# Kernel tuning notes

Hardware: AMD Instinct MI355X
Metric: run time of the kernel (lower is better)

The kernel has to match this reference:

```python
import jax, jax.numpy as jnp
import numpy as np
from jax import lax

C, HID, NCLS, CDIM = 16, 128, 32, 64

def _dwconv(x, k):
    # x: [B,C,H,W], k: [C,1,3,3] depthwise (groups=C), SAME padding
    return lax.conv_general_dilated(
        x, k, window_strides=(1, 1), padding='SAME',
        dimension_numbers=('NCHW', 'OIHW', 'NCHW'), feature_group_count=x.shape[1])

def setup_inputs() -> dict:
    key = jax.random.key(0)
    ks = jax.random.split(key, 10)
    B, H, W = 4, 256, 256
    Fin = 3 * C
    inp = {
        'x': jax.random.normal(ks[0], (B, C, H, W), jnp.float32),
        'cond': jax.random.randint(ks[1], (B,), 0, NCLS, jnp.int32),
        'embed': jax.random.normal(ks[2], (NCLS, CDIM), jnp.float32) * 0.1,
        # Linear weights stored as [in, out] (transposed torch layout)
        'film_w': jax.random.normal(ks[3], (CDIM, 2 * HID), jnp.float32) * (1.0 / np.sqrt(CDIM)),
        'film_b': jnp.zeros((2 * HID,), jnp.float32),
        'fc1_w': jax.random.normal(ks[4], (Fin, HID), jnp.float32) * (1.0 / np.sqrt(Fin)),
        'fc1_b': jnp.zeros((HID,), jnp.float32),
        'fc2_w': jax.random.normal(ks[5], (HID, HID), jnp.float32) * (1.0 / np.sqrt(HID)),
        'fc2_b': jnp.zeros((HID,), jnp.float32),
        # fc3 is zero-init in the module; use small random values so output != input
        'fc3_w': jax.random.normal(ks[6], (HID, C), jnp.float32) * 0.01,
        'fc3_b': jnp.zeros((C,), jnp.float32),
        'n_steps': 4,
    }
    return inp

def reference(x, cond, embed, film_w, film_b, fc1_w, fc1_b, fc2_w, fc2_b, fc3_w, fc3_b, n_steps):
    sx = jnp.array([[-1., 0., 1.], [-2., 0., 2.], [-1., 0., 1.]], jnp.float32)
    kx = jnp.tile(sx[None, None], (C, 1, 1, 1))   # [C,1,3,3]
    ky = jnp.tile(sx.T[None, None], (C, 1, 1, 1))

    # FiLM params are step-invariant: compute once
    film = embed[cond] @ film_w + film_b          # [B, 2*HID]
    gamma, beta = jnp.split(film, 2, axis=1)      # [B, HID] each
    gamma = gamma[:, None, None, :]               # [B,1,1,HID]
    beta = beta[:, None, None, :]

    def step(xs, _):
        gx = _dwconv(xs, kx)
        gy = _dwconv(xs, ky)
        feats = jnp.concatenate([xs, gx, gy], axis=1).transpose(0, 2, 3, 1)  # [B,H,W,3C]
        h = jax.nn.relu(feats @ fc1_w + fc1_b)
        h = gamma * h + beta
        h = jax.nn.relu(h @ fc2_w + fc2_b)
        dx = (h @ fc3_w + fc3_b).transpose(0, 3, 1, 2)                        # [B,C,H,W]
        dx = jnp.clip(dx, -10.0, 10.0)
        return xs + dx * 0.1, None

    out, _ = lax.scan(step, x, None, length=n_steps)
    return out
```

## Files before the change

### kernel.cpp

```cpp
#include <hip/hip_runtime.h>

typedef __bf16 bf16x8 __attribute__((ext_vector_type(8)));
typedef float f32x4 __attribute__((ext_vector_type(4)));
typedef float f32x16 __attribute__((ext_vector_type(16)));
typedef unsigned int u32x4 __attribute__((ext_vector_type(4)));

#define FILM_WS 0
#define W1_WS   4096
#define W2B_WS  20480
#define W3_WS   151552
#define B2_WS   159744
#define XBUF_WS 163840

#define W1_OFF  0
#define W2_OFF  16384
#define W3_OFF  49152
#define B2_OFF  57344
#define XL_OFF  57856
#define LDS_TOTAL 92672

static __device__ __forceinline__ unsigned short f2bf(float f) {
  unsigned int u = __builtin_bit_cast(unsigned int, f);
  u += 0x7fffu + ((u >> 16) & 1u);
  return (unsigned short)(u >> 16);
}

static __device__ __forceinline__ unsigned cvtpk(float lo, float hi) {
  unsigned r;
  asm("v_cvt_pk_bf16_f32 %0, %1, %2" : "=v"(r) : "v"(lo), "v"(hi));
  return r;
}

static __device__ __forceinline__ void plswap(unsigned &a, unsigned &b) {
  auto r = __builtin_amdgcn_permlane32_swap((int)a, (int)b, false, false);
  a = (unsigned)r[0];
  b = (unsigned)r[1];
}

__global__ __launch_bounds__(256) void prep_film(
    const int* __restrict__ cond, const float* __restrict__ embed,
    const float* __restrict__ film_w, const float* __restrict__ film_b,
    char* __restrict__ ws) {
  int id = blockIdx.x * 256 + threadIdx.x;
  int b = id >> 8, j = id & 255;
  const float* e = embed + cond[b] * 64;
  float s = film_b[j];
  #pragma unroll 8
  for (int k = 0; k < 64; ++k) s += e[k] * film_w[k * 256 + j];
  ((float*)(ws + FILM_WS))[b * 256 + j] = s;
}

__global__ __launch_bounds__(256) void prep_w(
    const float* __restrict__ fc1w, const float* __restrict__ fc1b,
    const float* __restrict__ fc2w, const float* __restrict__ fc2b,
    const float* __restrict__ fc3w, char* __restrict__ ws) {
  int id = blockIdx.x * 256 + threadIdx.x;
  const float* film = (const float*)(ws + FILM_WS);
  if (id < 8192) {
    int n = id >> 6, k = id & 63;
    float v = (k < 48) ? fc1w[k * 128 + n] : (k == 48 ? fc1b[n] : 0.f);
    *(unsigned short*)(ws + W1_WS + ((n * 128 + 2 * k) ^ ((n & 7) << 4))) = f2bf(v);
  } else if (id < 8192 + 65536) {
    int t = id - 8192; int bb = t >> 14; t &= 16383;
    int n = t >> 7, k = t & 127;
    float v = film[bb * 256 + k] * fc2w[k * 128 + n];
    *(unsigned short*)(ws + W2B_WS + bb * 32768 + ((n * 256 + 2 * k) ^ ((n & 15) << 4))) = f2bf(v);
  } else if (id < 8192 + 65536 + 4096) {
    int t = id - 73728; int n = t >> 7, k = t & 127;
    float v = (n < 16) ? fc3w[k * 16 + n] : 0.f;
    *(unsigned short*)(ws + W3_WS + ((n * 256 + 2 * k) ^ ((n & 15) << 4))) = f2bf(v);
  } else if (id < 8192 + 65536 + 4096 + 512) {
    int t = id - 77824; int bb = t >> 7, n = t & 127;
    float s = fc2b[n];
    for (int k = 0; k < 128; ++k)
      s += film[bb * 256 + 128 + k] * fc2w[k * 128 + n];
    ((float*)(ws + B2_WS))[bb * 128 + n] = s;
  }
}

__global__ __launch_bounds__(512, 2) void step_kernel(
    const float* __restrict__ xin, float* __restrict__ xout,
    const char* __restrict__ ws, const float* __restrict__ fc3b) {
  extern __shared__ char sm[];
  float* smf = (float*)(sm + XL_OFF);
  const int tid = threadIdx.x;
  const int bid = blockIdx.x;
  const int b = bid >> 6, idx = bid & 63;

  for (int i = tid; i < 3584; i += 512) {
    const char* src; int dst;
    if (i < 1024)      { src = ws + W1_WS + i * 16;                       dst = W1_OFF + i * 16; }
    else if (i < 3072) { src = ws + W2B_WS + b * 32768 + (i - 1024) * 16; dst = W2_OFF + (i - 1024) * 16; }
    else               { src = ws + W3_WS + (i - 3072) * 16;              dst = W3_OFF + (i - 3072) * 16; }
    *(u32x4*)(sm + dst) = *(const u32x4*)src;
  }
  if (tid < 128)
    ((float*)(sm + B2_OFF))[tid] = ((const float*)(ws + B2_WS + b * 512))[tid];

  const int lane = tid & 63, wv = tid >> 6;
  const int l31 = lane & 31, h5 = lane >> 5;
  const int band = wv * 32;
  const int p = band + l31, pr = p >> 7, pcol = p & 127;
  const int cbase = h5 * 8;
  const float b3v = (l31 < 16) ? fc3b[l31] : 0.f;
  const unsigned bONE = (h5 == 0) ? 0x3F80u : 0u;
  const bf16x8 fone = __builtin_bit_cast(bf16x8, (u32x4){bONE, 0u, 0u, 0u});

  const int iseg = tid >> 5, iq = tid & 31;
  const int eseg = tid >> 1, ee = tid & 1;

  f32x4 pre[4];
  float peg = 0.f;
  {
    const int h0 = idx * 4;
    #pragma unroll
    for (int k = 0; k < 4; ++k) {
      int seg = iseg + k * 16;
      int c = seg >> 2, dh = seg & 3;
      int g = h0 - 1 + dh;
      pre[k] = (f32x4){0.f, 0.f, 0.f, 0.f};
      if ((unsigned)g < 256u)
        pre[k] = *(const f32x4*)(xin + (((b * 16 + c) * 256 + g) << 8) + 4 * iq);
    }
    if (tid < 128) {
      int c = eseg >> 2, dh = eseg & 3;
      int g = h0 - 1 + dh;
      int w = -1 + ee * 129;
      if ((unsigned)g < 256u && (unsigned)w < 256u)
        peg = xin[(((b * 16 + c) * 256 + g) << 8) + w];
    }
  }

  for (int j = 0; j < 4; ++j) {
    const int h0 = idx * 4 + (j >> 1) * 2;
    const int w0 = (j & 1) << 7;
    __syncthreads();
    #pragma unroll
    for (int k = 0; k < 4; ++k)
      *(f32x4*)(smf + (iseg + k * 16) * 136 + 4 + 4 * iq) = pre[k];
    if (tid < 128)
      smf[eseg * 136 + 3 + ee * 129] = peg;
    __syncthreads();

    if (j < 3) {
      const int nh0 = idx * 4 + ((j + 1) >> 1) * 2;
      const int nw0 = ((j + 1) & 1) << 7;
      #pragma unroll
      for (int k = 0; k < 4; ++k) {
        int seg = iseg + k * 16;
        int c = seg >> 2, dh = seg & 3;
        int g = nh0 - 1 + dh;
        pre[k] = (f32x4){0.f, 0.f, 0.f, 0.f};
        if ((unsigned)g < 256u)
          pre[k] = *(const f32x4*)(xin + (((b * 16 + c) * 256 + g) << 8) + nw0 + 4 * iq);
      }
      peg = 0.f;
      if (tid < 128) {
        int c = eseg >> 2, dh = eseg & 3;
        int g = nh0 - 1 + dh;
        int w = nw0 - 1 + ee * 129;
        if ((unsigned)g < 256u && (unsigned)w < 256u)
          peg = xin[(((b * 16 + c) * 256 + g) << 8) + w];
      }
    }

    bf16x8 fx, fgx, fgy;
    #pragma unroll
    for (int jc = 0; jc < 8; ++jc) {
      const float* s0 = smf + ((cbase + jc) * 4 + pr) * 136 + 3 + pcol;
      float a00 = s0[0],   a01 = s0[1],   a02 = s0[2];
      float a10 = s0[136], a11 = s0[137], a12 = s0[138];
      float a20 = s0[272], a21 = s0[273], a22 = s0[274];
      fx[jc]  = (__bf16)a11;
      fgx[jc] = (__bf16)((a02 - a00) + 2.f * (a12 - a10) + (a22 - a20));
      fgy[jc] = (__bf16)((a20 - a00) + 2.f * (a21 - a01) + (a22 - a02));
    }

    f32x16 acc1[4];
    #pragma unroll
    for (int nt = 0; nt < 4; ++nt) {
      const int n = nt * 32 + l31;
      const int rb = n * 128, sw = (n & 7) << 4;
      bf16x8 wA = __builtin_bit_cast(bf16x8, *(const u32x4*)(sm + W1_OFF + ((rb +  0 + 16 * h5) ^ sw)));
      bf16x8 wB = __builtin_bit_cast(bf16x8, *(const u32x4*)(sm + W1_OFF + ((rb + 32 + 16 * h5) ^ sw)));
      bf16x8 wC = __builtin_bit_cast(bf16x8, *(const u32x4*)(sm + W1_OFF + ((rb + 64 + 16 * h5) ^ sw)));
      bf16x8 wD = __builtin_bit_cast(bf16x8, *(const u32x4*)(sm + W1_OFF + ((rb + 96 + 16 * h5) ^ sw)));
      f32x16 a = (f32x16){0.f,0.f,0.f,0.f,0.f,0.f,0.f,0.f,0.f,0.f,0.f,0.f,0.f,0.f,0.f,0.f};
      a = __builtin_amdgcn_mfma_f32_32x32x16_bf16(wA, fx,   a, 0, 0, 0);
      a = __builtin_amdgcn_mfma_f32_32x32x16_bf16(wB, fgx,  a, 0, 0, 0);
      a = __builtin_amdgcn_mfma_f32_32x32x16_bf16(wC, fgy,  a, 0, 0, 0);
      a = __builtin_amdgcn_mfma_f32_32x32x16_bf16(wD, fone, a, 0, 0, 0);
      acc1[nt] = a;
    }

    unsigned zf[8][4];
    #pragma unroll
    for (int kk = 0; kk < 8; ++kk) {
      const int Qa = 2 * kk, Qb = 2 * kk + 1;
      unsigned A0 = cvtpk(fmaxf(acc1[Qa >> 2][(Qa & 3) * 4 + 0], 0.f),
                          fmaxf(acc1[Qa >> 2][(Qa & 3) * 4 + 1], 0.f));
      unsigned A1 = cvtpk(fmaxf(acc1[Qa >> 2][(Qa & 3) * 4 + 2], 0.f),
                          fmaxf(acc1[Qa >> 2][(Qa & 3) * 4 + 3], 0.f));
      unsigned B0 = cvtpk(fmaxf(acc1[Qb >> 2][(Qb & 3) * 4 + 0], 0.f),
                          fmaxf(acc1[Qb >> 2][(Qb & 3) * 4 + 1], 0.f));
      unsigned B1 = cvtpk(fmaxf(acc1[Qb >> 2][(Qb & 3) * 4 + 2], 0.f),
                          fmaxf(acc1[Qb >> 2][(Qb & 3) * 4 + 3], 0.f));
      plswap(A0, B0); plswap(A1, B1);
      zf[kk][0] = A0; zf[kk][1] = A1; zf[kk][2] = B0; zf[kk][3] = B1;
    }

    float bv[4];
    #pragma unroll
    for (int nt = 0; nt < 4; ++nt)
      bv[nt] = ((const float*)(sm + B2_OFF))[nt * 32 + l31];
    f32x16 acc2[4];
    #pragma unroll
    for (int nt = 0; nt < 4; ++nt) {
      const int n = nt * 32 + l31;
      const int rb = n * 256, sw = (n & 15) << 4;
      f32x16 a = (f32x16){0.f,0.f,0.f,0.f,0.f,0.f,0.f,0.f,0.f,0.f,0.f,0.f,0.f,0.f,0.f,0.f};
      #pragma unroll
      for (int kk = 0; kk < 8; ++kk) {
        bf16x8 wf = __builtin_bit_cast(bf16x8,
            *(const u32x4*)(sm + W2_OFF + ((rb + 32 * kk + 16 * h5) ^ sw)));
        bf16x8 zk = __builtin_bit_cast(bf16x8,
            (u32x4){zf[kk][0], zf[kk][1], zf[kk][2], zf[kk][3]});
        a = __builtin_amdgcn_mfma_f32_32x32x16_bf16(wf, zk, a, 0, 0, 0);
      }
      bf16x8 wb = __builtin_bit_cast(bf16x8,
          (u32x4){(h5 == 0) ? cvtpk(bv[nt], 0.f) : 0u, 0u, 0u, 0u});
      a = __builtin_amdgcn_mfma_f32_32x32x16_bf16(wb, fone, a, 0, 0, 0);
      acc2[nt] = a;
    }

    unsigned hf[8][4];
    #pragma unroll
    for (int kk = 0; kk < 8; ++kk) {
      const int Qa = 2 * kk, Qb = 2 * kk + 1;
      unsigned A0 = cvtpk(fmaxf(acc2[Qa >> 2][(Qa & 3) * 4 + 0], 0.f),
                          fmaxf(acc2[Qa >> 2][(Qa & 3) * 4 + 1], 0.f));
      unsigned A1 = cvtpk(fmaxf(acc2[Qa >> 2][(Qa & 3) * 4 + 2], 0.f),
                          fmaxf(acc2[Qa >> 2][(Qa & 3) * 4 + 3], 0.f));
      unsigned B0 = cvtpk(fmaxf(acc2[Qb >> 2][(Qb & 3) * 4 + 0], 0.f),
                          fmaxf(acc2[Qb >> 2][(Qb & 3) * 4 + 1], 0.f));
      unsigned B1 = cvtpk(fmaxf(acc2[Qb >> 2][(Qb & 3) * 4 + 2], 0.f),
                          fmaxf(acc2[Qb >> 2][(Qb & 3) * 4 + 3], 0.f));
      plswap(A0, B0); plswap(A1, B1);
      hf[kk][0] = A0; hf[kk][1] = A1; hf[kk][2] = B0; hf[kk][3] = B1;
    }

    f32x16 a3 = (f32x16){0.f,0.f,0.f,0.f,0.f,0.f,0.f,0.f,0.f,0.f,0.f,0.f,0.f,0.f,0.f,0.f};
    {
      const int rb = l31 * 256, sw = (l31 & 15) << 4;
      #pragma unroll
      for (int kk = 0; kk < 8; ++kk) {
        bf16x8 wf = __builtin_bit_cast(bf16x8,
            *(const u32x4*)(sm + W3_OFF + ((rb + 32 * kk + 16 * h5) ^ sw)));
        bf16x8 hk = __builtin_bit_cast(bf16x8,
            (u32x4){hf[kk][0], hf[kk][1], hf[kk][2], hf[kk][3]});
        a3 = __builtin_amdgcn_mfma_f32_32x32x16_bf16(wf, hk, a3, 0, 0, 0);
      }
      bf16x8 wb = __builtin_bit_cast(bf16x8,
          (u32x4){(h5 == 0) ? cvtpk(b3v, 0.f) : 0u, 0u, 0u, 0u});
      a3 = __builtin_amdgcn_mfma_f32_32x32x16_bf16(wb, fone, a3, 0, 0, 0);
    }

    #pragma unroll
    for (int r = 0; r < 8; ++r) {
      const int c = 4 * h5 + (r & 3) + 8 * (r >> 2);
      float dx = a3[r];
      dx = fminf(fmaxf(dx, -10.f), 10.f);
      float xold = smf[(c * 4 + pr + 1) * 136 + 4 + pcol];
      xout[(((b * 16 + c) * 256 + h0 + pr) << 8) + w0 + pcol] = xold + 0.1f * dx;
    }
  }
}

extern "C" void kernel_launch(void* const* d_in, const int* in_sizes, int n_in,
                              void* d_out, int out_size, void* d_ws, size_t ws_size,
                              hipStream_t stream) {
  const float* x      = (const float*)d_in[0];
  const int*   cond   = (const int*)d_in[1];
  const float* embed  = (const float*)d_in[2];
  const float* film_w = (const float*)d_in[3];
  const float* film_b = (const float*)d_in[4];
  const float* fc1w   = (const float*)d_in[5];
  const float* fc1b   = (const float*)d_in[6];
  const float* fc2w   = (const float*)d_in[7];
  const float* fc2b   = (const float*)d_in[8];
  const float* fc3w   = (const float*)d_in[9];
  const float* fc3b   = (const float*)d_in[10];

  char*  ws   = (char*)d_ws;
  float* xbuf = (float*)(ws + XBUF_WS);
  float* out  = (float*)d_out;

  prep_film<<<4, 256, 0, stream>>>(cond, embed, film_w, film_b, ws);
  prep_w<<<306, 256, 0, stream>>>(fc1w, fc1b, fc2w, fc2b, fc3w, ws);

  dim3 grid(256), blk(512);
  step_kernel<<<grid, blk, LDS_TOTAL, stream>>>(x,    xbuf, ws, fc3b);
  step_kernel<<<grid, blk, LDS_TOTAL, stream>>>(xbuf, out,  ws, fc3b);
  step_kernel<<<grid, blk, LDS_TOTAL, stream>>>(out,  xbuf, ws, fc3b);
  step_kernel<<<grid, blk, LDS_TOTAL, stream>>>(xbuf, out,  ws, fc3b);
}
```

Baseline: 107.5 us.

## Process two pixel tiles per wave with a taller 6-row halo tile

Each wave now handles 64 pixels as two 32-pixel MFMA column tiles, so every weight fragment loaded from LDS feeds two MFMAs. The block tile is 4 rows by 128 columns with a 6-row halo, processed in two passes instead of four passes of 2 rows, which cuts redundant halo loads and barriers. The bias values move from LDS into registers preloaded once, and the accumulator-to-bf16 conversion is interleaved per n-tile. In exchange, LDS grows to about 107 KB and register pressure roughly doubles, which may limit occupancy under the 2-blocks-per-CU launch bound.

After: 178.3 us. 1.66x slower.

```diff
diff --git a/kernel.cpp b/kernel.cpp
--- a/kernel.cpp
+++ b/kernel.cpp
@@ -15,9 +15,8 @@
 #define W1_OFF  0
 #define W2_OFF  16384
 #define W3_OFF  49152
-#define B2_OFF  57344
-#define XL_OFF  57856
-#define LDS_TOTAL 92672
+#define XL_OFF  57344
+#define LDS_TOTAL 109568
 
 static __device__ __forceinline__ unsigned short f2bf(float f) {
   unsigned int u = __builtin_bit_cast(unsigned int, f);
@@ -36,6 +35,23 @@
   a = (unsigned)r[0];
   b = (unsigned)r[1];
 }
+
+#define CVTSTORE(Z, nt, a) do {                                          \
+    unsigned A0 = cvtpk(fmaxf((a)[0], 0.f),  fmaxf((a)[1], 0.f));        \
+    unsigned A1 = cvtpk(fmaxf((a)[2], 0.f),  fmaxf((a)[3], 0.f));        \
+    unsigned B0 = cvtpk(fmaxf((a)[4], 0.f),  fmaxf((a)[5], 0.f));        \
+    unsigned B1 = cvtpk(fmaxf((a)[6], 0.f),  fmaxf((a)[7], 0.f));        \
+    plswap(A0, B0); plswap(A1, B1);                                      \
+    Z[2*(nt)][0] = A0; Z[2*(nt)][1] = A1; Z[2*(nt)][2] = B0; Z[2*(nt)][3] = B1; \
+    A0 = cvtpk(fmaxf((a)[8], 0.f),  fmaxf((a)[9], 0.f));                 \
+    A1 = cvtpk(fmaxf((a)[10], 0.f), fmaxf((a)[11], 0.f));                \
+    B0 = cvtpk(fmaxf((a)[12], 0.f), fmaxf((a)[13], 0.f));                \
+    B1 = cvtpk(fmaxf((a)[14], 0.f), fmaxf((a)[15], 0.f));                \
+    plswap(A0, B0); plswap(A1, B1);                                      \
+    Z[2*(nt)+1][0] = A0; Z[2*(nt)+1][1] = A1; Z[2*(nt)+1][2] = B0; Z[2*(nt)+1][3] = B1; \
+  } while (0)
+
+#define ZERO16 (f32x16){0.f,0.f,0.f,0.f,0.f,0.f,0.f,0.f,0.f,0.f,0.f,0.f,0.f,0.f,0.f,0.f}
 
 __global__ __launch_bounds__(256) void prep_film(
     const int* __restrict__ cond, const float* __restrict__ embed,
@@ -86,6 +102,7 @@
   const int tid = threadIdx.x;
   const int bid = blockIdx.x;
   const int b = bid >> 6, idx = bid & 63;
+  const int h0 = idx * 4;
 
   for (int i = tid; i < 3584; i += 512) {
     const char* src; int dst;
@@ -94,89 +111,90 @@
     else               { src = ws + W3_WS + (i - 3072) * 16;              dst = W3_OFF + (i - 3072) * 16; }
     *(u32x4*)(sm + dst) = *(const u32x4*)src;
   }
-  if (tid < 128)
-    ((float*)(sm + B2_OFF))[tid] = ((const float*)(ws + B2_WS + b * 512))[tid];
 
   const int lane = tid & 63, wv = tid >> 6;
   const int l31 = lane & 31, h5 = lane >> 5;
-  const int band = wv * 32;
-  const int p = band + l31, pr = p >> 7, pcol = p & 127;
+  const int band = wv * 64;
+  const int p0 = band + l31,      p1 = band + 32 + l31;
+  const int pr0 = p0 >> 7, pc0 = p0 & 127;
+  const int pr1 = p1 >> 7, pc1 = p1 & 127;
   const int cbase = h5 * 8;
-  const float b3v = (l31 < 16) ? fc3b[l31] : 0.f;
   const unsigned bONE = (h5 == 0) ? 0x3F80u : 0u;
   const bf16x8 fone = __builtin_bit_cast(bf16x8, (u32x4){bONE, 0u, 0u, 0u});
 
+  unsigned wb2[4];
+  #pragma unroll
+  for (int nt = 0; nt < 4; ++nt) {
+    float bvv = ((const float*)(ws + B2_WS))[b * 128 + nt * 32 + l31];
+    wb2[nt] = (h5 == 0) ? cvtpk(bvv, 0.f) : 0u;
+  }
+  const float b3v = (l31 < 16) ? fc3b[l31] : 0.f;
+  const unsigned wb3 = (h5 == 0) ? cvtpk(b3v, 0.f) : 0u;
+
   const int iseg = tid >> 5, iq = tid & 31;
   const int eseg = tid >> 1, ee = tid & 1;
 
-  f32x4 pre[4];
-  float peg = 0.f;
-  {
-    const int h0 = idx * 4;
-    #pragma unroll
-    for (int k = 0; k < 4; ++k) {
-      int seg = iseg + k * 16;
-      int c = seg >> 2, dh = seg & 3;
+  f32x4 pre[6];
+  float peg;
+  auto PREFETCH = [&](int w0p) {
+    #pragma unroll
+    for (int k = 0; k < 6; ++k) {
+      int seg = iseg + 16 * k;
+      int c = seg / 6, dh = seg - 6 * c;
       int g = h0 - 1 + dh;
       pre[k] = (f32x4){0.f, 0.f, 0.f, 0.f};
       if ((unsigned)g < 256u)
-        pre[k] = *(const f32x4*)(xin + (((b * 16 + c) * 256 + g) << 8) + 4 * iq);
-    }
-    if (tid < 128) {
-      int c = eseg >> 2, dh = eseg & 3;
+        pre[k] = *(const f32x4*)(xin + (((b * 16 + c) * 256 + g) << 8) + w0p + 4 * iq);
+    }
+    peg = 0.f;
+    if (tid < 192) {
+      int c = eseg / 6, dh = eseg - 6 * c;
       int g = h0 - 1 + dh;
-      int w = -1 + ee * 129;
+      int w = w0p - 1 + ee * 129;
       if ((unsigned)g < 256u && (unsigned)w < 256u)
         peg = xin[(((b * 16 + c) * 256 + g) << 8) + w];
     }
-  }
-
-  for (int j = 0; j < 4; ++j) {
-    const int h0 = idx * 4 + (j >> 1) * 2;
-    const int w0 = (j & 1) << 7;
+  };
+
+  PREFETCH(0);
+
+  #pragma unroll
+  for (int j = 0; j < 2; ++j) {
+    const int w0 = j << 7;
     __syncthreads();
     #pragma unroll
-    for (int k = 0; k < 4; ++k)
-      *(f32x4*)(smf + (iseg + k * 16) * 136 + 4 + 4 * iq) = pre[k];
-    if (tid < 128)
+    for (int k = 0; k < 6; ++k)
+      *(f32x4*)(smf + (iseg + 16 * k) * 136 + 4 + 4 * iq) = pre[k];
+    if (tid < 192)
       smf[eseg * 136 + 3 + ee * 129] = peg;
     __syncthreads();
 
-    if (j < 3) {
-      const int nh0 = idx * 4 + ((j + 1) >> 1) * 2;
-      const int nw0 = ((j + 1) & 1) << 7;
-      #pragma unroll
-      for (int k = 0; k < 4; ++k) {
-        int seg = iseg + k * 16;
-        int c = seg >> 2, dh = seg & 3;
-        int g = nh0 - 1 + dh;
-        pre[k] = (f32x4){0.f, 0.f, 0.f, 0.f};
-        if ((unsigned)g < 256u)
-          pre[k] = *(const f32x4*)(xin + (((b * 16 + c) * 256 + g) << 8) + nw0 + 4 * iq);
-      }
-      peg = 0.f;
-      if (tid < 128) {
-        int c = eseg >> 2, dh = eseg & 3;
-        int g = nh0 - 1 + dh;
-        int w = nw0 - 1 + ee * 129;
-        if ((unsigned)g < 256u && (unsigned)w < 256u)
-          peg = xin[(((b * 16 + c) * 256 + g) << 8) + w];
-      }
-    }
-
-    bf16x8 fx, fgx, fgy;
+    if (j == 0) PREFETCH(128);
+
+    bf16x8 fx0, fgx0, fgy0, fx1, fgx1, fgy1;
     #pragma unroll
     for (int jc = 0; jc < 8; ++jc) {
-      const float* s0 = smf + ((cbase + jc) * 4 + pr) * 136 + 3 + pcol;
-      float a00 = s0[0],   a01 = s0[1],   a02 = s0[2];
-      float a10 = s0[136], a11 = s0[137], a12 = s0[138];
-      float a20 = s0[272], a21 = s0[273], a22 = s0[274];
-      fx[jc]  = (__bf16)a11;
-      fgx[jc] = (__bf16)((a02 - a00) + 2.f * (a12 - a10) + (a22 - a20));
-      fgy[jc] = (__bf16)((a20 - a00) + 2.f * (a21 - a01) + (a22 - a02));
-    }
-
-    f32x16 acc1[4];
+      {
+        const float* s0 = smf + ((cbase + jc) * 6 + pr0) * 136 + 3 + pc0;
+        float a00 = s0[0],   a01 = s0[1],   a02 = s0[2];
+        float a10 = s0[136], a11 = s0[137], a12 = s0[138];
+        float a20 = s0[272], a21 = s0[273], a22 = s0[274];
+        fx0[jc]  = (__bf16)a11;
+        fgx0[jc] = (__bf16)((a02 - a00) + 2.f * (a12 - a10) + (a22 - a20));
+        fgy0[jc] = (__bf16)((a20 - a00) + 2.f * (a21 - a01) + (a22 - a02));
+      }
+      {
+        const float* s0 = smf + ((cbase + jc) * 6 + pr1) * 136 + 3 + pc1;
+        float a00 = s0[0],   a01 = s0[1],   a02 = s0[2];
+        float a10 = s0[136], a11 = s0[137], a12 = s0[138];
+        float a20 = s0[272], a21 = s0[273], a22 = s0[274];
+        fx1[jc]  = (__bf16)a11;
+        fgx1[jc] = (__bf16)((a02 - a00) + 2.f * (a12 - a10) + (a22 - a20));
+        fgy1[jc] = (__bf16)((a20 - a00) + 2.f * (a21 - a01) + (a22 - a02));
+      }
+    }
+
+    unsigned zf0[8][4], zf1[8][4];
     #pragma unroll
     for (int nt = 0; nt < 4; ++nt) {
       const int n = nt * 32 + l31;
@@ -185,93 +203,67 @@
       bf16x8 wB = __builtin_bit_cast(bf16x8, *(const u32x4*)(sm + W1_OFF + ((rb + 32 + 16 * h5) ^ sw)));
       bf16x8 wC = __builtin_bit_cast(bf16x8, *(const u32x4*)(sm + W1_OFF + ((rb + 64 + 16 * h5) ^ sw)));
       bf16x8 wD = __builtin_bit_cast(bf16x8, *(const u32x4*)(sm + W1_OFF + ((rb + 96 + 16 * h5) ^ sw)));
-      f32x16 a = (f32x16){0.f,0.f,0.f,0.f,0.f,0.f,0.f,0.f,0.f,0.f,0.f,0.f,0.f,0.f,0.f,0.f};
-      a = __builtin_amdgcn_mfma_f32_32x32x16_bf16(wA, fx,   a, 0, 0, 0);
-      a = __builtin_amdgcn_mfma_f32_32x32x16_bf16(wB, fgx,  a, 0, 0, 0);
-      a = __builtin_amdgcn_mfma_f32_32x32x16_bf16(wC, fgy,  a, 0, 0, 0);
-      a = __builtin_amdgcn_mfma_f32_32x32x16_bf16(wD, fone, a, 0, 0, 0);
-      acc1[nt] = a;
-    }
-
-    unsigned zf[8][4];
-    #pragma unroll
-    for (int kk = 0; kk < 8; ++kk) {
-      const int Qa = 2 * kk, Qb = 2 * kk + 1;
-      unsigned A0 = cvtpk(fmaxf(acc1[Qa >> 2][(Qa & 3) * 4 + 0], 0.f),
-                          fmaxf(acc1[Qa >> 2][(Qa & 3) * 4 + 1], 0.f));
-      unsigned A1 = cvtpk(fmaxf(acc1[Qa >> 2][(Qa & 3) * 4 + 2], 0.f),
-                          fmaxf(acc1[Qa >> 2][(Qa & 3) * 4 + 3], 0.f));
-      unsigned B0 = cvtpk(fmaxf(acc1[Qb >> 2][(Qb & 3) * 4 + 0], 0.f),
-                          fmaxf(acc1[Qb >> 2][(Qb & 3) * 4 + 1], 0.f));
-      unsigned B1 = cvtpk(fmaxf(acc1[Qb >> 2][(Qb & 3) * 4 + 2], 0.f),
-                          fmaxf(acc1[Qb >> 2][(Qb & 3) * 4 + 3], 0.f));
-      plswap(A0, B0); plswap(A1, B1);
-      zf[kk][0] = A0; zf[kk][1] = A1; zf[kk][2] = B0; zf[kk][3] = B1;
-    }
-
-    float bv[4];
-    #pragma unroll
-    for (int nt = 0; nt < 4; ++nt)
-      bv[nt] = ((const float*)(sm + B2_OFF))[nt * 32 + l31];
-    f32x16 acc2[4];
+      f32x16 a0 = ZERO16, a1 = ZERO16;
+      a0 = __builtin_amdgcn_mfma_f32_32x32x16_bf16(wA, fx0,  a0, 0, 0, 0);
+      a1 = __builtin_amdgcn_mfma_f32_32x32x16_bf16(wA, fx1,  a1, 0, 0, 0);
+      a0 = __builtin_amdgcn_mfma_f32_32x32x16_bf16(wB, fgx0, a0, 0, 0, 0);
+      a1 = __builtin_amdgcn_mfma_f32_32x32x16_bf16(wB, fgx1, a1, 0, 0, 0);
+      a0 = __builtin_amdgcn_mfma_f32_32x32x16_bf16(wC, fgy0, a0, 0, 0, 0);
+      a1 = __builtin_amdgcn_mfma_f32_32x32x16_bf16(wC, fgy1, a1, 0, 0, 0);
+      a0 = __builtin_amdgcn_mfma_f32_32x32x16_bf16(wD, fone, a0, 0, 0, 0);
+      a1 = __builtin_amdgcn_mfma_f32_32x32x16_bf16(wD, fone, a1, 0, 0, 0);
+      CVTSTORE(zf0, nt, a0);
+      CVTSTORE(zf1, nt, a1);
+    }
+
+    unsigned hf0[8][4], hf1[8][4];
     #pragma unroll
     for (int nt = 0; nt < 4; ++nt) {
       const int n = nt * 32 + l31;
       const int rb = n * 256, sw = (n & 15) << 4;
-      f32x16 a = (f32x16){0.f,0.f,0.f,0.f,0.f,0.f,0.f,0.f,0.f,0.f,0.f,0.f,0.f,0.f,0.f,0.f};
+      f32x16 a0 = ZERO16, a1 = ZERO16;
       #pragma unroll
       for (int kk = 0; kk < 8; ++kk) {
         bf16x8 wf = __builtin_bit_cast(bf16x8,
             *(const u32x4*)(sm + W2_OFF + ((rb + 32 * kk + 16 * h5) ^ sw)));
-        bf16x8 zk = __builtin_bit_cast(bf16x8,
-            (u32x4){zf[kk][0], zf[kk][1], zf[kk][2], zf[kk][3]});
-        a = __builtin_amdgcn_mfma_f32_32x32x16_bf16(wf, zk, a, 0, 0, 0);
-      }
-      bf16x8 wb = __builtin_bit_cast(bf16x8,
-          (u32x4){(h5 == 0) ? cvtpk(bv[nt], 0.f) : 0u, 0u, 0u, 0u});
-      a = __builtin_amdgcn_mfma_f32_32x32x16_bf16(wb, fone, a, 0, 0, 0);
-      acc2[nt] = a;
-    }
-
-    unsigned hf[8][4];
-    #pragma unroll
-    for (int kk = 0; kk < 8; ++kk) {
-      const int Qa = 2 * kk, Qb = 2 * kk + 1;
-      unsigned A0 = cvtpk(fmaxf(acc2[Qa >> 2][(Qa & 3) * 4 + 0], 0.f),
-                          fmaxf(acc2[Qa >> 2][(Qa & 3) * 4 + 1], 0.f));
-      unsigned A1 = cvtpk(fmaxf(acc2[Qa >> 2][(Qa & 3) * 4 + 2], 0.f),
-                          fmaxf(acc2[Qa >> 2][(Qa & 3) * 4 + 3], 0.f));
-      unsigned B0 = cvtpk(fmaxf(acc2[Qb >> 2][(Qb & 3) * 4 + 0], 0.f),
-                          fmaxf(acc2[Qb >> 2][(Qb & 3) * 4 + 1], 0.f));
-      unsigned B1 = cvtpk(fmaxf(acc2[Qb >> 2][(Qb & 3) * 4 + 2], 0.f),
-                          fmaxf(acc2[Qb >> 2][(Qb & 3) * 4 + 3], 0.f));
-      plswap(A0, B0); plswap(A1, B1);
-      hf[kk][0] = A0; hf[kk][1] = A1; hf[kk][2] = B0; hf[kk][3] = B1;
-    }
-
-    f32x16 a3 = (f32x16){0.f,0.f,0.f,0.f,0.f,0.f,0.f,0.f,0.f,0.f,0.f,0.f,0.f,0.f,0.f,0.f};
+        a0 = __builtin_amdgcn_mfma_f32_32x32x16_bf16(wf,
+            __builtin_bit_cast(bf16x8, (u32x4){zf0[kk][0], zf0[kk][1], zf0[kk][2], zf0[kk][3]}), a0, 0, 0, 0);
+        a1 = __builtin_amdgcn_mfma_f32_32x32x16_bf16(wf,
+            __builtin_bit_cast(bf16x8, (u32x4){zf1[kk][0], zf1[kk][1], zf1[kk][2], zf1[kk][3]}), a1, 0, 0, 0);
+      }
+      bf16x8 wbf = __builtin_bit_cast(bf16x8, (u32x4){wb2[nt], 0u, 0u, 0u});
+      a0 = __builtin_amdgcn_mfma_f32_32x32x16_bf16(wbf, fone, a0, 0, 0, 0);
+      a1 = __builtin_amdgcn_mfma_f32_32x32x16_bf16(wbf, fone, a1, 0, 0, 0);
+      CVTSTORE(hf0, nt, a0);
+      CVTSTORE(hf1, nt, a1);
+    }
+
+    f32x16 c0 = ZERO16, c1 = ZERO16;
     {
       const int rb = l31 * 256, sw = (l31 & 15) << 4;
       #pragma unroll
       for (int kk = 0; kk < 8; ++kk) {
         bf16x8 wf = __builtin_bit_cast(bf16x8,
             *(const u32x4*)(sm + W3_OFF + ((rb + 32 * kk + 16 * h5) ^ sw)));
-        bf16x8 hk = __builtin_bit_cast(bf16x8,
-            (u32x4){hf[kk][0], hf[kk][1], hf[kk][2], hf[kk][3]});
-        a3 = __builtin_amdgcn_mfma_f32_32x32x16_bf16(wf, hk, a3, 0, 0, 0);
-      }
-      bf16x8 wb = __builtin_bit_cast(bf16x8,
-          (u32x4){(h5 == 0) ? cvtpk(b3v, 0.f) : 0u, 0u, 0u, 0u});
-      a3 = __builtin_amdgcn_mfma_f32_32x32x16_bf16(wb, fone, a3, 0, 0, 0);
+        c0 = __builtin_amdgcn_mfma_f32_32x32x16_bf16(wf,
+            __builtin_bit_cast(bf16x8, (u32x4){hf0[kk][0], hf0[kk][1], hf0[kk][2], hf0[kk][3]}), c0, 0, 0, 0);
+        c1 = __builtin_amdgcn_mfma_f32_32x32x16_bf16(wf,
+            __builtin_bit_cast(bf16x8, (u32x4){hf1[kk][0], hf1[kk][1], hf1[kk][2], hf1[kk][3]}), c1, 0, 0, 0);
+      }
+      bf16x8 wbf = __builtin_bit_cast(bf16x8, (u32x4){wb3, 0u, 0u, 0u});
+      c0 = __builtin_amdgcn_mfma_f32_32x32x16_bf16(wbf, fone, c0, 0, 0, 0);
+      c1 = __builtin_amdgcn_mfma_f32_32x32x16_bf16(wbf, fone, c1, 0, 0, 0);
     }
 
     #pragma unroll
     for (int r = 0; r < 8; ++r) {
       const int c = 4 * h5 + (r & 3) + 8 * (r >> 2);
-      float dx = a3[r];
-      dx = fminf(fmaxf(dx, -10.f), 10.f);
-      float xold = smf[(c * 4 + pr + 1) * 136 + 4 + pcol];
-      xout[(((b * 16 + c) * 256 + h0 + pr) << 8) + w0 + pcol] = xold + 0.1f * dx;
+      float dx0 = fminf(fmaxf(c0[r], -10.f), 10.f);
+      float xo0 = smf[(c * 6 + pr0 + 1) * 136 + 4 + pc0];
+      xout[(((b * 16 + c) * 256 + h0 + pr0) << 8) + w0 + pc0] = xo0 + 0.1f * dx0;
+      float dx1 = fminf(fmaxf(c1[r], -10.f), 10.f);
+      float xo1 = smf[(c * 6 + pr1 + 1) * 136 + 4 + pc1];
+      xout[(((b * 16 + c) * 256 + h0 + pr1) << 8) + w0 + pc1] = xo1 + 0.1f * dx1;
     }
   }
 }
```
